# Kernel tuning notes

Hardware: AMD Instinct MI355X
Metric: run time of the kernel (lower is better)

## Reference

```python
import math
import jax, jax.numpy as jnp
from jax import lax
import numpy as np

D = 128            # head_dim
B = 16             # independent KV streams (e.g., heads)
S = 4096           # update sequence length
P = 4096           # reconstruction positions
MAX_SEQ_LEN = 8192
# (n_waves, ema_rate, freq_low, freq_high) per level, coarse -> fine
LEVELS = [(16, 0.001, 0.01, 1.0), (32, 0.005, 0.5, 3.0), (64, 0.02, 1.0, 6.0), (128, 0.05, 2.0, 10.0), (256, 0.1, 4.0, 20.0)]
TWO_PI = 2.0 * math.pi


def setup_inputs() -> dict:
    key = jax.random.key(0)
    ks = jax.random.split(key, 2 + len(LEVELS))
    inp = {}
    inp['kv_vectors'] = jax.random.normal(ks[0], (B, S, D), dtype=jnp.float32)
    inp['positions'] = jnp.arange(S, dtype=jnp.int32)
    inp['recon_positions'] = jnp.sort(jax.random.randint(ks[1], (P,), 0, MAX_SEQ_LEN, dtype=jnp.int32))
    for i, (n, a, lo, hi) in enumerate(LEVELS):
        k1, k2 = jax.random.split(ks[2 + i], 2)
        inp[f'W_enc_{i}'] = jax.random.normal(k1, (3 * n, D), dtype=jnp.float32) / math.sqrt(D)
        inp[f'W_dec_{i}'] = jax.random.normal(k2, (D, n), dtype=jnp.float32) / math.sqrt(n)
        inp[f'base_freqs_{i}'] = jnp.linspace(lo, hi, n, dtype=jnp.float32)
    return inp


def _ema_final(x, alpha):
    # x: [S, ...]; returns EMA state after S sequential steps from zero init.
    def step(c, xt):
        return (1.0 - alpha) * c + alpha * xt, None
    final, _ = lax.scan(step, jnp.zeros(x.shape[1:], x.dtype), x)
    return final


def _forward(kv_vectors, positions, recon_positions, params):
    pos_norm = positions.astype(jnp.float32)[:, None] / MAX_SEQ_LEN    # [S,1]
    rpos_norm = recon_positions.astype(jnp.float32)[:, None] / MAX_SEQ_LEN  # [P,1]
    out = jnp.zeros((kv_vectors.shape[0], recon_positions.shape[0], D), jnp.float32)
    for (n, alpha, _lo, _hi), (W_enc, W_dec, base_freqs) in zip(LEVELS, params):
        deltas = jnp.einsum('bsd,wd->bsw', kv_vectors, W_enc)          # [B,S,3n]
        d_freq, d_amp, d_phase = jnp.split(deltas, 3, axis=-1)         # each [B,S,n]
        pos_signal = jnp.sin(base_freqs[None, :] * pos_norm * TWO_PI)  # [S,n]
        xs = jnp.stack([d_freq * pos_signal[None], jnp.abs(d_amp), d_phase], axis=0)  # [3,B,S,n]
        xs = jnp.transpose(xs, (2, 0, 1, 3))                           # [S,3,B,n]
        freqs, amps, phases = _ema_final(xs, alpha)                    # each [B,n]
        wave_phases = TWO_PI * (freqs[:, None, :] + base_freqs[None, None, :]) * rpos_norm[None] + phases[:, None, :]
        wave_values = amps[:, None, :] * jnp.sin(wave_phases)          # [B,P,n]
        out = out + jnp.einsum('bpn,dn->bpd', wave_values, W_dec)
    return out


def reference(kv_vectors, positions, recon_positions,
              W_enc_0, W_dec_0, base_freqs_0,
              W_enc_1, W_dec_1, base_freqs_1,
              W_enc_2, W_dec_2, base_freqs_2,
              W_enc_3, W_dec_3, base_freqs_3,
              W_enc_4, W_dec_4, base_freqs_4):
    params = [(W_enc_0, W_dec_0, base_freqs_0), (W_enc_1, W_dec_1, base_freqs_1),
              (W_enc_2, W_dec_2, base_freqs_2), (W_enc_3, W_dec_3, base_freqs_3),
              (W_enc_4, W_dec_4, base_freqs_4)]
    return _forward(kv_vectors, positions, recon_positions, params)
```

## Files before the change

kernel.cpp:

```cpp
#include <hip/hip_runtime.h>

typedef __attribute__((ext_vector_type(8))) short short8;
typedef __attribute__((ext_vector_type(4))) float floatx4;

#define B_   16
#define S_   4096
#define D_   128
#define P_   4096
#define CTOT 496
#define BP   (B_ * CTOT)
#define WPADG 512
#define CENC 1488
#define INV2PI 0.15915494309189535f

__device__ __forceinline__ unsigned short f2bf(float f) {
    unsigned u = __float_as_uint(f);
    u += 0x7fffu + ((u >> 16) & 1u);
    return (unsigned short)(u >> 16);
}
__device__ __forceinline__ unsigned int pack2(float a, float b) {
    return (unsigned int)f2bf(a) | ((unsigned int)f2bf(b) << 16);
}

#define NKVB 4096
#define NWB  1000
#define NZB  93
__global__ void pack_all(const float* __restrict__ kv,
                         const float* __restrict__ we0, const float* __restrict__ we1,
                         const float* __restrict__ we2, const float* __restrict__ we3,
                         const float* __restrict__ we4,
                         const float* __restrict__ wd0, const float* __restrict__ wd1,
                         const float* __restrict__ wd2, const float* __restrict__ wd3,
                         const float* __restrict__ wd4,
                         unsigned short* __restrict__ kvb16,
                         unsigned short* __restrict__ wencb,
                         unsigned short* __restrict__ wdbT,
                         float* __restrict__ accb)
{
    const int bid = blockIdx.x, tid = threadIdx.x;
    if (bid < NKVB) {
        size_t base = ((size_t)bid * 256 + tid) * 8;
        float4 a = *(const float4*)(kv + base);
        float4 c = *(const float4*)(kv + base + 4);
        union { unsigned int u[4]; short8 s; } r;
        r.u[0] = pack2(a.x, a.y); r.u[1] = pack2(a.z, a.w);
        r.u[2] = pack2(c.x, c.y); r.u[3] = pack2(c.z, c.w);
        *(short8*)(kvb16 + base) = r.s;
    } else if (bid < NKVB + NWB) {
        int idx = (bid - NKVB) * 256 + tid;
        const int NE = CENC * D_;
        if (idx < NE) {
            int c = idx >> 7, d = idx & 127;
            const float* src; int off;
            if (c < 48)        { src = we0; off = 0;   }
            else if (c < 144)  { src = we1; off = 48;  }
            else if (c < 336)  { src = we2; off = 144; }
            else               { src = (c < 720) ? we3 : we4; off = (c < 720) ? 336 : 720; }
            wencb[idx] = f2bf(src[(size_t)(c - off) * D_ + d]);
        } else {
            int k = idx - NE;
            int d = k >> 9, w = k & 511;
            float v = 0.0f;
            if (w < CTOT) {
                const float* src; int off, nl;
                if (w < 16)       { src = wd0; off = 0;   nl = 16;  }
                else if (w < 48)  { src = wd1; off = 16;  nl = 32;  }
                else if (w < 112) { src = wd2; off = 48;  nl = 64;  }
                else if (w < 240) { src = wd3; off = 112; nl = 128; }
                else              { src = wd4; off = 240; nl = 256; }
                v = src[(size_t)d * nl + (w - off)];
            }
            wdbT[k] = f2bf(v);
        }
    } else {
        int idx = (bid - NKVB - NWB) * 256 + tid;
        if (idx < 3 * BP) accb[idx] = 0.0f;
    }
}

__global__ __launch_bounds__(256) void encoder(
    const unsigned short* __restrict__ kvb16, const int* __restrict__ positions,
    const unsigned short* __restrict__ wencb,
    const float* __restrict__ bfr0, const float* __restrict__ bfr1,
    const float* __restrict__ bfr2, const float* __restrict__ bfr3,
    const float* __restrict__ bfr4,
    float* __restrict__ accb)
{
    const int b    = blockIdx.y;
    const int gw   = blockIdx.x * 4 + (threadIdx.x >> 6);
    const int lane = threadIdx.x & 63, ln15 = lane & 15, quad = lane >> 4;

    int bx, widx, nw;
    if (gw < 96)       { bx = gw / 24;                widx = gw % 24;      nw = 24; }
    else if (gw < 144) { int r = gw - 96;  bx = 4 + r / 12;  widx = r % 12; nw = 12; }
    else if (gw < 192) { int r = gw - 144; bx = 8 + r / 6;   widx = r % 6;  nw = 6;  }
    else               { int r = gw - 192; bx = 16 + r / 2;  widx = r % 2;  nw = 2;  }
    const int t0  = S_ - 64 * (bx + 1);
    const int sz2 = (bx < 16) ? 12 : 0, sz3 = (bx < 8) ? 24 : 0;
    const int cnt = 9 + sz2 + sz3 + ((bx < 4) ? 48 : 0);

    const unsigned short* abase = kvb16 + ((size_t)(b * S_ + t0 + ln15)) * D_ + quad * 8;
    short8 afr[4][4];
    #pragma unroll
    for (int m = 0; m < 4; ++m)
        #pragma unroll
        for (int k = 0; k < 4; ++k)
            afr[m][k] = *(const short8*)(abase + (m * 16) * D_ + k * 32);

    float pfr[16];
    #pragma unroll
    for (int m = 0; m < 4; ++m) {
        int4 pi = *(const int4*)(positions + t0 + m * 16 + quad * 4);
        pfr[m * 4 + 0] = (float)pi.x * (1.0f / 8192.0f);
        pfr[m * 4 + 1] = (float)pi.y * (1.0f / 8192.0f);
        pfr[m * 4 + 2] = (float)pi.z * (1.0f / 8192.0f);
        pfr[m * 4 + 3] = (float)pi.w * (1.0f / 8192.0f);
    }

    const int   n_l[5]  = {16, 32, 64, 128, 256};
    const int   coff[5] = {0, 16, 48, 112, 240};
    const int   c3[5]   = {0, 48, 144, 336, 720};
    const float al[5]   = {0.001f, 0.005f, 0.02f, 0.05f, 0.1f};
    const float l2m[5]  = {-0.0014434169f, -0.0072315692f, -0.0291463449f,
                           -0.0740005794f, -0.1520030934f};
    const float* bfp[5] = {bfr0, bfr1, bfr2, bfr3, bfr4};

    int   lprev = -1;
    float wtr[16];

    for (int ch = widx; ch < cnt; ch += nw) {
        int c = ch, l = 0;
        if (c >= 3) { c -= 3; l = 1;
            if (c >= 6) { c -= 6; l = 2;
                if (c >= sz2) { c -= sz2; l = 3;
                    if (c >= sz3) { c -= sz3; l = 4; } } } }
        const int ci = c, n = n_l[l];

        if (l != lprev) {
            lprev = l;
            const float s1 = (float)(S_ - 1 - t0);
            #pragma unroll
            for (int i = 0; i < 16; ++i) {
                float trel = (float)((i >> 2) * 16 + quad * 4 + (i & 3));
                wtr[i] = al[l] * exp2f((s1 - trel) * l2m[l]);
            }
        }

        const unsigned short* wrow = wencb + (size_t)(c3[l] + ci * 16 + ln15) * D_ + quad * 8;
        floatx4 acc[4];
        #pragma unroll
        for (int m = 0; m < 4; ++m) acc[m] = (floatx4){0.f, 0.f, 0.f, 0.f};
        #pragma unroll
        for (int k = 0; k < 4; ++k) {
            short8 bfg = *(const short8*)(wrow + k * 32);
            #pragma unroll
            for (int m = 0; m < 4; ++m)
                acc[m] = __builtin_amdgcn_mfma_f32_16x16x32_bf16(afr[m][k], bfg, acc[m], 0, 0, 0);
        }

        const int kind  = (ci * 16) / n;
        const int local = ci * 16 + ln15 - kind * n;
        const float bsv = (kind == 0) ? bfp[l][local] : 0.0f;
        float s = 0.0f;
        #pragma unroll
        for (int m = 0; m < 4; ++m)
            #pragma unroll
            for (int r = 0; r < 4; ++r) {
                float v = acc[m][r];
                if (kind == 0) {
                    float rev = bsv * pfr[m * 4 + r];
                    rev -= floorf(rev);
                    v *= __builtin_amdgcn_sinf(rev);
                } else if (kind == 1) {
                    v = fabsf(v);
                }
                s += wtr[m * 4 + r] * v;
            }
        s += __shfl_xor(s, 16);
        s += __shfl_xor(s, 32);
        if (lane < 16)
            atomicAdd(accb + (size_t)kind * BP + b * CTOT + coff[l] + local, s);
    }
}

__global__ __launch_bounds__(256) void decoder(
    const float* __restrict__ accb,
    const float* __restrict__ b0, const float* __restrict__ b1,
    const float* __restrict__ b2, const float* __restrict__ b3,
    const float* __restrict__ b4,
    const unsigned short* __restrict__ wdbT, const int* __restrict__ rpos,
    float* __restrict__ out)
{
    __shared__ unsigned short v[64 * 264];
    __shared__ float rpn[64];
    const int b = blockIdx.y, p0 = blockIdx.x * 64, tid = threadIdx.x;
    if (tid < 64) rpn[tid] = (float)rpos[p0 + tid] * (1.0f / 8192.0f);

    float Qv[2], Av[2], Pv[2];
    #pragma unroll
    for (int h = 0; h < 2; ++h) {
        int w = h * 256 + tid;
        float A = 0.f, Q = 0.f, P = 0.f;
        if (w < CTOT) {
            const float* bf; int off;
            if (w < 16)       { bf = b0; off = 0;   }
            else if (w < 48)  { bf = b1; off = 16;  }
            else if (w < 112) { bf = b2; off = 48;  }
            else if (w < 240) { bf = b3; off = 112; }
            else              { bf = b4; off = 240; }
            float f  = accb[0 * BP + b * CTOT + w];
            A        = accb[1 * BP + b * CTOT + w];
            float ph = accb[2 * BP + b * CTOT + w];
            Q = f + bf[w - off];
            P = ph * INV2PI;
        }
        Qv[h] = Q; Av[h] = A; Pv[h] = P;
    }

    const int wid = tid >> 6, lane = tid & 63, ln = lane & 15, quad = lane >> 4;
    const int nt0 = wid * 2;

    floatx4 acc[4][2];
    #pragma unroll
    for (int m = 0; m < 4; ++m)
        #pragma unroll
        for (int j = 0; j < 2; ++j) acc[m][j] = (floatx4){0.f, 0.f, 0.f, 0.f};

    #pragma unroll
    for (int half = 0; half < 2; ++half) {
        const int w0 = half * 256;
        const float Q = Qv[half], A = Av[half], Ph = Pv[half];
        __syncthreads();
        for (int p = 0; p < 64; ++p) {
            float r = fmaf(Q, rpn[p], Ph);
            r -= floorf(r);
            v[p * 264 + tid] = f2bf(A * __builtin_amdgcn_sinf(r));
        }
        __syncthreads();

        #pragma unroll
        for (int kk = 0; kk < 8; ++kk) {
            short8 bn[2];
            #pragma unroll
            for (int j = 0; j < 2; ++j)
                bn[j] = *(const short8*)(wdbT + (size_t)((nt0 + j) * 16 + ln) * WPADG
                                         + w0 + kk * 32 + quad * 8);
            short8 am[4];
            #pragma unroll
            for (int m = 0; m < 4; ++m)
                am[m] = *(const short8*)&v[(m * 16 + ln) * 264 + kk * 32 + quad * 8];
            #pragma unroll
            for (int m = 0; m < 4; ++m)
                #pragma unroll
                for (int j = 0; j < 2; ++j)
                    acc[m][j] = __builtin_amdgcn_mfma_f32_16x16x32_bf16(
                                    am[m], bn[j], acc[m][j], 0, 0, 0);
        }
    }

    #pragma unroll
    for (int m = 0; m < 4; ++m)
        #pragma unroll
        for (int j = 0; j < 2; ++j)
            #pragma unroll
            for (int r = 0; r < 4; ++r) {
                int p = p0 + m * 16 + quad * 4 + r;
                int d = (nt0 + j) * 16 + ln;
                out[((size_t)(b * P_ + p)) * D_ + d] = acc[m][j][r];
            }
}

extern "C" void kernel_launch(void* const* d_in, const int* in_sizes, int n_in,
                              void* d_out, int out_size, void* d_ws, size_t ws_size,
                              hipStream_t stream)
{
    const float* kv        = (const float*)d_in[0];
    const int*   positions = (const int*)d_in[1];
    const int*   rpos      = (const int*)d_in[2];

    char* ws = (char*)d_ws;
    float*          accb  = (float*)(ws + 0);
    unsigned short* wencb = (unsigned short*)(ws + 95232);
    unsigned short* wdbT  = (unsigned short*)(ws + 476160);
    unsigned short* kvb16 = (unsigned short*)(ws + 607232);

    pack_all<<<NKVB + NWB + NZB, 256, 0, stream>>>(
        kv,
        (const float*)d_in[3], (const float*)d_in[6], (const float*)d_in[9],
        (const float*)d_in[12], (const float*)d_in[15],
        (const float*)d_in[4], (const float*)d_in[7], (const float*)d_in[10],
        (const float*)d_in[13], (const float*)d_in[16],
        kvb16, wencb, wdbT, accb);

    encoder<<<dim3(72, B_), 256, 0, stream>>>(
        kvb16, positions, wencb,
        (const float*)d_in[5], (const float*)d_in[8], (const float*)d_in[11],
        (const float*)d_in[14], (const float*)d_in[17],
        accb);

    decoder<<<dim3(P_ / 64, B_), 256, 0, stream>>>(
        accb,
        (const float*)d_in[5], (const float*)d_in[8], (const float*)d_in[11],
        (const float*)d_in[14], (const float*)d_in[17],
        wdbT, rpos, (float*)d_out);
}
```

Baseline: 173.5 us.

## Fuse bf16 packing into encoder and drop separate pack kernel

Removes the pack_all kernel. kv and W_enc are now converted to bf16 on the fly inside the encoder as they are loaded, W_dec packing moves into the blockIdx.y==0 blocks of the encoder, and accb is zeroed with hipMemsetAsync. The encoder grid shrinks from 72 to 33 blocks per stream, so each wave handles more channel chunks. This avoids a full fp32 read plus bf16 write of kv (about 32MB of memory traffic) and one launch. The cost is fewer waves in flight and redundant fp32 weight loads and conversions inside each wave.

```diff
diff --git a/kernel.cpp b/kernel.cpp
--- a/kernel.cpp
+++ b/kernel.cpp
@@ -10,8 +10,9 @@
 #define CTOT 496
 #define BP   (B_ * CTOT)
 #define WPADG 512
-#define CENC 1488
 #define INV2PI 0.15915494309189535f
+#define NWAVE_B 132
+#define NJB 33
 
 __device__ __forceinline__ unsigned short f2bf(float f) {
     unsigned u = __float_as_uint(f);
@@ -22,108 +23,78 @@
     return (unsigned int)f2bf(a) | ((unsigned int)f2bf(b) << 16);
 }
 
-#define NKVB 4096
-#define NWB  1000
-#define NZB  93
-__global__ void pack_all(const float* __restrict__ kv,
-                         const float* __restrict__ we0, const float* __restrict__ we1,
-                         const float* __restrict__ we2, const float* __restrict__ we3,
-                         const float* __restrict__ we4,
-                         const float* __restrict__ wd0, const float* __restrict__ wd1,
-                         const float* __restrict__ wd2, const float* __restrict__ wd3,
-                         const float* __restrict__ wd4,
-                         unsigned short* __restrict__ kvb16,
-                         unsigned short* __restrict__ wencb,
-                         unsigned short* __restrict__ wdbT,
-                         float* __restrict__ accb)
+__global__ __launch_bounds__(256) void encoder(
+    const float* __restrict__ kv, const int* __restrict__ positions,
+    const float* __restrict__ we0, const float* __restrict__ we1,
+    const float* __restrict__ we2, const float* __restrict__ we3,
+    const float* __restrict__ we4,
+    const float* __restrict__ wd0, const float* __restrict__ wd1,
+    const float* __restrict__ wd2, const float* __restrict__ wd3,
+    const float* __restrict__ wd4,
+    const float* __restrict__ bf0, const float* __restrict__ bf1,
+    const float* __restrict__ bf2, const float* __restrict__ bf3,
+    const float* __restrict__ bf4,
+    float* __restrict__ accb,
+    unsigned short* __restrict__ wdbT)
 {
-    const int bid = blockIdx.x, tid = threadIdx.x;
-    if (bid < NKVB) {
-        size_t base = ((size_t)bid * 256 + tid) * 8;
-        float4 a = *(const float4*)(kv + base);
-        float4 c = *(const float4*)(kv + base + 4);
-        union { unsigned int u[4]; short8 s; } r;
-        r.u[0] = pack2(a.x, a.y); r.u[1] = pack2(a.z, a.w);
-        r.u[2] = pack2(c.x, c.y); r.u[3] = pack2(c.z, c.w);
-        *(short8*)(kvb16 + base) = r.s;
-    } else if (bid < NKVB + NWB) {
-        int idx = (bid - NKVB) * 256 + tid;
-        const int NE = CENC * D_;
-        if (idx < NE) {
-            int c = idx >> 7, d = idx & 127;
-            const float* src; int off;
-            if (c < 48)        { src = we0; off = 0;   }
-            else if (c < 144)  { src = we1; off = 48;  }
-            else if (c < 336)  { src = we2; off = 144; }
-            else               { src = (c < 720) ? we3 : we4; off = (c < 720) ? 336 : 720; }
-            wencb[idx] = f2bf(src[(size_t)(c - off) * D_ + d]);
-        } else {
-            int k = idx - NE;
-            int d = k >> 9, w = k & 511;
-            float v = 0.0f;
-            if (w < CTOT) {
+    const int tid = threadIdx.x;
+
+    if (blockIdx.y == 0) {
+        int g = blockIdx.x * 256 + tid;
+        int k0 = g * 8;
+        if (k0 < D_ * WPADG) {
+            int d = k0 >> 9, w0g = k0 & 511;
+            union { unsigned int u[4]; short8 s; } r;
+            if (w0g >= CTOT) {
+                r.u[0] = r.u[1] = r.u[2] = r.u[3] = 0;
+            } else {
                 const float* src; int off, nl;
-                if (w < 16)       { src = wd0; off = 0;   nl = 16;  }
-                else if (w < 48)  { src = wd1; off = 16;  nl = 32;  }
-                else if (w < 112) { src = wd2; off = 48;  nl = 64;  }
-                else if (w < 240) { src = wd3; off = 112; nl = 128; }
-                else              { src = wd4; off = 240; nl = 256; }
-                v = src[(size_t)d * nl + (w - off)];
-            }
-            wdbT[k] = f2bf(v);
-        }
-    } else {
-        int idx = (bid - NKVB - NWB) * 256 + tid;
-        if (idx < 3 * BP) accb[idx] = 0.0f;
-    }
-}
-
-__global__ __launch_bounds__(256) void encoder(
-    const unsigned short* __restrict__ kvb16, const int* __restrict__ positions,
-    const unsigned short* __restrict__ wencb,
-    const float* __restrict__ bfr0, const float* __restrict__ bfr1,
-    const float* __restrict__ bfr2, const float* __restrict__ bfr3,
-    const float* __restrict__ bfr4,
-    float* __restrict__ accb)
-{
+                if (w0g < 16)       { src = wd0; off = 0;   nl = 16;  }
+                else if (w0g < 48)  { src = wd1; off = 16;  nl = 32;  }
+                else if (w0g < 112) { src = wd2; off = 48;  nl = 64;  }
+                else if (w0g < 240) { src = wd3; off = 112; nl = 128; }
+                else                { src = wd4; off = 240; nl = 256; }
+                const float* p = src + (size_t)d * nl + (w0g - off);
+                float4 a = *(const float4*)(p);
+                float4 c = *(const float4*)(p + 4);
+                r.u[0] = pack2(a.x, a.y); r.u[1] = pack2(a.z, a.w);
+                r.u[2] = pack2(c.x, c.y); r.u[3] = pack2(c.z, c.w);
+            }
+            *(short8*)(wdbT + k0) = r.s;
+        }
+    }
+
     const int b    = blockIdx.y;
-    const int gw   = blockIdx.x * 4 + (threadIdx.x >> 6);
-    const int lane = threadIdx.x & 63, ln15 = lane & 15, quad = lane >> 4;
+    const int rem  = blockIdx.x * 4 + (tid >> 6);
+    const int lane = tid & 63, ln15 = lane & 15, quad = lane >> 4;
 
     int bx, widx, nw;
-    if (gw < 96)       { bx = gw / 24;                widx = gw % 24;      nw = 24; }
-    else if (gw < 144) { int r = gw - 96;  bx = 4 + r / 12;  widx = r % 12; nw = 12; }
-    else if (gw < 192) { int r = gw - 144; bx = 8 + r / 6;   widx = r % 6;  nw = 6;  }
-    else               { int r = gw - 192; bx = 16 + r / 2;  widx = r % 2;  nw = 2;  }
+    if (rem < 40)      { bx = rem / 10;               widx = rem % 10; nw = 10; }
+    else if (rem < 60) { int r = rem - 40; bx = 4 + r / 5; widx = r % 5; nw = 5; }
+    else if (rem < 84) { int r = rem - 60; bx = 8 + r / 3; widx = r % 3; nw = 3; }
+    else               { bx = 16 + (rem - 84);        widx = 0;        nw = 1; }
     const int t0  = S_ - 64 * (bx + 1);
-    const int sz2 = (bx < 16) ? 12 : 0, sz3 = (bx < 8) ? 24 : 0;
-    const int cnt = 9 + sz2 + sz3 + ((bx < 4) ? 48 : 0);
-
-    const unsigned short* abase = kvb16 + ((size_t)(b * S_ + t0 + ln15)) * D_ + quad * 8;
+    const int cnt = (bx < 4) ? 93 : (bx < 8) ? 45 : (bx < 16) ? 21 : 9;
+
+    const float* arow = kv + ((size_t)(b * S_ + t0 + ln15)) * D_ + quad * 8;
     short8 afr[4][4];
     #pragma unroll
     for (int m = 0; m < 4; ++m)
         #pragma unroll
-        for (int k = 0; k < 4; ++k)
-            afr[m][k] = *(const short8*)(abase + (m * 16) * D_ + k * 32);
-
-    float pfr[16];
-    #pragma unroll
-    for (int m = 0; m < 4; ++m) {
-        int4 pi = *(const int4*)(positions + t0 + m * 16 + quad * 4);
-        pfr[m * 4 + 0] = (float)pi.x * (1.0f / 8192.0f);
-        pfr[m * 4 + 1] = (float)pi.y * (1.0f / 8192.0f);
-        pfr[m * 4 + 2] = (float)pi.z * (1.0f / 8192.0f);
-        pfr[m * 4 + 3] = (float)pi.w * (1.0f / 8192.0f);
-    }
+        for (int k = 0; k < 4; ++k) {
+            float4 x = *(const float4*)(arow + m * 16 * D_ + k * 32);
+            float4 y = *(const float4*)(arow + m * 16 * D_ + k * 32 + 4);
+            union { unsigned int u[4]; short8 s; } r;
+            r.u[0] = pack2(x.x, x.y); r.u[1] = pack2(x.z, x.w);
+            r.u[2] = pack2(y.x, y.y); r.u[3] = pack2(y.z, y.w);
+            afr[m][k] = r.s;
+        }
 
     const int   n_l[5]  = {16, 32, 64, 128, 256};
     const int   coff[5] = {0, 16, 48, 112, 240};
-    const int   c3[5]   = {0, 48, 144, 336, 720};
     const float al[5]   = {0.001f, 0.005f, 0.02f, 0.05f, 0.1f};
     const float l2m[5]  = {-0.0014434169f, -0.0072315692f, -0.0291463449f,
                            -0.0740005794f, -0.1520030934f};
-    const float* bfp[5] = {bfr0, bfr1, bfr2, bfr3, bfr4};
 
     int   lprev = -1;
     float wtr[16];
@@ -132,8 +103,8 @@
         int c = ch, l = 0;
         if (c >= 3) { c -= 3; l = 1;
             if (c >= 6) { c -= 6; l = 2;
-                if (c >= sz2) { c -= sz2; l = 3;
-                    if (c >= sz3) { c -= sz3; l = 4; } } } }
+                if (c >= 12) { c -= 12; l = 3;
+                    if (c >= 24) { c -= 24; l = 4; } } } }
         const int ci = c, n = n_l[l];
 
         if (l != lprev) {
@@ -146,36 +117,57 @@
             }
         }
 
-        const unsigned short* wrow = wencb + (size_t)(c3[l] + ci * 16 + ln15) * D_ + quad * 8;
+        const float* wel = (l == 0) ? we0 : (l == 1) ? we1 :
+                           (l == 2) ? we2 : (l == 3) ? we3 : we4;
+        const float* wrow = wel + (size_t)(ci * 16 + ln15) * D_ + quad * 8;
+
         floatx4 acc[4];
         #pragma unroll
         for (int m = 0; m < 4; ++m) acc[m] = (floatx4){0.f, 0.f, 0.f, 0.f};
         #pragma unroll
         for (int k = 0; k < 4; ++k) {
-            short8 bfg = *(const short8*)(wrow + k * 32);
-            #pragma unroll
-            for (int m = 0; m < 4; ++m)
-                acc[m] = __builtin_amdgcn_mfma_f32_16x16x32_bf16(afr[m][k], bfg, acc[m], 0, 0, 0);
+            float4 x = *(const float4*)(wrow + k * 32);
+            float4 y = *(const float4*)(wrow + k * 32 + 4);
+            union { unsigned int u[4]; short8 s; } r;
+            r.u[0] = pack2(x.x, x.y); r.u[1] = pack2(x.z, x.w);
+            r.u[2] = pack2(y.x, y.y); r.u[3] = pack2(y.z, y.w);
+            #pragma unroll
+            for (int m = 0; m < 4; ++m)
+                acc[m] = __builtin_amdgcn_mfma_f32_16x16x32_bf16(
+                             afr[m][k], r.s, acc[m], 0, 0, 0);
         }
 
         const int kind  = (ci * 16) / n;
         const int local = ci * 16 + ln15 - kind * n;
-        const float bsv = (kind == 0) ? bfp[l][local] : 0.0f;
         float s = 0.0f;
-        #pragma unroll
-        for (int m = 0; m < 4; ++m)
-            #pragma unroll
-            for (int r = 0; r < 4; ++r) {
-                float v = acc[m][r];
-                if (kind == 0) {
-                    float rev = bsv * pfr[m * 4 + r];
+        if (kind == 0) {
+            const float* bfl = (l == 0) ? bf0 : (l == 1) ? bf1 :
+                               (l == 2) ? bf2 : (l == 3) ? bf3 : bf4;
+            const float bsv = bfl[local];
+            #pragma unroll
+            for (int m = 0; m < 4; ++m) {
+                int4 pi = *(const int4*)(positions + t0 + m * 16 + quad * 4);
+                float pfv[4] = {(float)pi.x, (float)pi.y, (float)pi.z, (float)pi.w};
+                #pragma unroll
+                for (int r = 0; r < 4; ++r) {
+                    float rev = bsv * pfv[r] * (1.0f / 8192.0f);
                     rev -= floorf(rev);
-                    v *= __builtin_amdgcn_sinf(rev);
-                } else if (kind == 1) {
-                    v = fabsf(v);
+                    s += wtr[m * 4 + r] * acc[m][r] * __builtin_amdgcn_sinf(rev);
                 }
-                s += wtr[m * 4 + r] * v;
-            }
+            }
+        } else if (kind == 1) {
+            #pragma unroll
+            for (int m = 0; m < 4; ++m)
+                #pragma unroll
+                for (int r = 0; r < 4; ++r)
+                    s += wtr[m * 4 + r] * fabsf(acc[m][r]);
+        } else {
+            #pragma unroll
+            for (int m = 0; m < 4; ++m)
+                #pragma unroll
+                for (int r = 0; r < 4; ++r)
+                    s += wtr[m * 4 + r] * acc[m][r];
+        }
         s += __shfl_xor(s, 16);
         s += __shfl_xor(s, 32);
         if (lane < 16)
@@ -202,16 +194,16 @@
         int w = h * 256 + tid;
         float A = 0.f, Q = 0.f, P = 0.f;
         if (w < CTOT) {
-            const float* bf; int off;
-            if (w < 16)       { bf = b0; off = 0;   }
-            else if (w < 48)  { bf = b1; off = 16;  }
-            else if (w < 112) { bf = b2; off = 48;  }
-            else if (w < 240) { bf = b3; off = 112; }
-            else              { bf = b4; off = 240; }
+            const float* bfl; int off;
+            if (w < 16)       { bfl = b0; off = 0;   }
+            else if (w < 48)  { bfl = b1; off = 16;  }
+            else if (w < 112) { bfl = b2; off = 48;  }
+            else if (w < 240) { bfl = b3; off = 112; }
+            else              { bfl = b4; off = 240; }
             float f  = accb[0 * BP + b * CTOT + w];
             A        = accb[1 * BP + b * CTOT + w];
             float ph = accb[2 * BP + b * CTOT + w];
-            Q = f + bf[w - off];
+            Q = f + bfl[w - off];
             P = ph * INV2PI;
         }
         Qv[h] = Q; Av[h] = A; Pv[h] = P;
@@ -279,24 +271,20 @@
     const int*   rpos      = (const int*)d_in[2];
 
     char* ws = (char*)d_ws;
-    float*          accb  = (float*)(ws + 0);
-    unsigned short* wencb = (unsigned short*)(ws + 95232);
-    unsigned short* wdbT  = (unsigned short*)(ws + 476160);
-    unsigned short* kvb16 = (unsigned short*)(ws + 607232);
-
-    pack_all<<<NKVB + NWB + NZB, 256, 0, stream>>>(
-        kv,
+    float*          accb = (float*)(ws + 0);
+    unsigned short* wdbT = (unsigned short*)(ws + 95232);
+
+    hipMemsetAsync(accb, 0, (size_t)(3 * BP) * sizeof(float), stream);
+
+    encoder<<<dim3(NJB, B_), 256, 0, stream>>>(
+        kv, positions,
         (const float*)d_in[3], (const float*)d_in[6], (const float*)d_in[9],
         (const float*)d_in[12], (const float*)d_in[15],
         (const float*)d_in[4], (const float*)d_in[7], (const float*)d_in[10],
         (const float*)d_in[13], (const float*)d_in[16],
-        kvb16, wencb, wdbT, accb);
-
-    encoder<<<dim3(72, B_), 256, 0, stream>>>(
-        kvb16, positions, wencb,
         (const float*)d_in[5], (const float*)d_in[8], (const float*)d_in[11],
         (const float*)d_in[14], (const float*)d_in[17],
-        accb);
+        accb, wdbT);
 
     decoder<<<dim3(P_ / 64, B_), 256, 0, stream>>>(
         accb,
```

Result: slower. 180.2 us (+3.9%).
